# Optimization experiments

Hardware: AMD Instinct MI355X
Metric: run time of the kernel (lower is better)

## Reference

```python
import jax, jax.numpy as jnp
import numpy as np

N = 20000      # total nodes (20 proteins x 1000 residues)
E = 320000     # edges (avg degree 16)
F_IN = 22      # amino-acid feature dim
H = 4          # attention heads
C = 64         # hidden dim per head
HC = H * C     # 256
G = 20         # number of graphs
OUT = 128      # output embedding dim
NEG_SLOPE = 0.2


def setup_inputs() -> dict:
    key = jax.random.key(0)
    ks = jax.random.split(key, 24)
    x = jax.random.normal(ks[0], (N, F_IN), dtype=jnp.float32)
    edge_index = jax.random.randint(ks[1], (2, E), 0, N)
    batch = jnp.arange(N, dtype=jnp.int64) // (N // G)  # 1000 nodes per graph
    s = 0.1
    d = {
        'x': x, 'edge_index': edge_index, 'batch': batch,
        'Win': jax.random.normal(ks[2], (F_IN, C)) * s,
        'bin_': jnp.zeros((C,), jnp.float32),
        'Wout': jax.random.normal(ks[3], (2 * HC, OUT)) * s,
        'bout': jnp.zeros((OUT,), jnp.float32),
    }
    kidx = 4
    for i in range(3):
        in_dim = C if i == 0 else HC
        d[f'Wl{i}'] = jax.random.normal(ks[kidx], (in_dim, HC)) * s; kidx += 1
        d[f'Wr{i}'] = jax.random.normal(ks[kidx], (in_dim, HC)) * s; kidx += 1
        d[f'att{i}'] = jax.random.normal(ks[kidx], (H, C)) * s; kidx += 1
        d[f'b{i}'] = jnp.zeros((HC,), jnp.float32)
    return d


def _gatv2_layer(h, src, dst, Wl, Wr, att, bias):
    # PyG GATv2Conv (share_weights=False, concat=True), dropout off (eval)
    xl = (h @ Wl).reshape(-1, H, C)   # source transform (x_j)
    xr = (h @ Wr).reshape(-1, H, C)   # target transform (x_i)
    e = jax.nn.leaky_relu(xl[src] + xr[dst], NEG_SLOPE)  # [E+N, H, C]
    logit = jnp.einsum('ehc,hc->eh', e, att)             # [E+N, H]
    mx = jax.ops.segment_max(logit, dst, num_segments=N)
    mx = jnp.where(jnp.isfinite(mx), mx, 0.0)
    ex = jnp.exp(logit - mx[dst])
    den = jax.ops.segment_sum(ex, dst, num_segments=N)
    alpha = ex / (den[dst] + 1e-16)                      # segment softmax
    out = jax.ops.segment_sum(alpha[:, :, None] * xl[src], dst, num_segments=N)
    return out.reshape(-1, HC) + bias


def reference(x, edge_index, batch, Win, bin_,
              Wl0, Wr0, att0, b0, Wl1, Wr1, att1, b1, Wl2, Wr2, att2, b2,
              Wout, bout):
    # add self-loops once (add_self_loops=True in every GATv2Conv)
    loops = jnp.arange(N, dtype=edge_index.dtype)
    src = jnp.concatenate([edge_index[0], loops])
    dst = jnp.concatenate([edge_index[1], loops])

    h = jax.nn.relu(x @ Win + bin_)  # input_proj + ReLU (dropout = eval identity)
    layers = [(Wl0, Wr0, att0, b0), (Wl1, Wr1, att1, b1), (Wl2, Wr2, att2, b2)]
    for (Wl, Wr, att, b) in layers:
        h_prev = h
        h = jax.nn.elu(_gatv2_layer(h, src, dst, Wl, Wr, att, b))
        if h_prev.shape[-1] == h.shape[-1]:  # residual when dims match (layers 1,2)
            h = h + h_prev

    counts = jax.ops.segment_sum(jnp.ones((N,), h.dtype), batch, num_segments=G)
    x_mean = jax.ops.segment_sum(h, batch, num_segments=G) / counts[:, None]
    x_max = jax.ops.segment_max(h, batch, num_segments=G)
    x_global = jnp.concatenate([x_mean, x_max], axis=-1)  # [G, 512]
    return x_global @ Wout + bout                          # [G, 128]
```

## Files before the change

kernel.cpp:

```cpp
#include <hip/hip_runtime.h>
#include <hip/hip_bf16.h>
#include <math.h>

#define N_NODES 20000
#define N_EDGES 320000
#define F_IN 22
#define H_HEADS 4
#define C_DIM 64
#define HC 256
#define G_GRAPHS 20
#define OUT_DIM 128
#define NODES_PER_G 1000
#define ELL_CAP 64
#define SCAT_NB ((N_EDGES + 255) / 256)
#define INPROJ_NB (N_NODES / 4)

#if __has_builtin(__builtin_amdgcn_exp2f)
#define EXP2F __builtin_amdgcn_exp2f
#else
#define EXP2F exp2f
#endif

typedef unsigned short ushortT;
typedef __attribute__((ext_vector_type(8))) short short8;
typedef __attribute__((ext_vector_type(4))) float v4f;
typedef __attribute__((ext_vector_type(2))) float f2;

typedef const __attribute__((address_space(1))) void* gas_p;
typedef __attribute__((address_space(3))) void* las_p;

__device__ inline ushortT f2bf(float f) {
    unsigned int u = __float_as_uint(f);
    unsigned int r = (u + 0x7fffu + ((u >> 16) & 1u)) >> 16;
    return (ushortT)r;
}

__device__ inline unsigned int fkey(float f) {
    unsigned int u = __float_as_uint(f);
    return ((int)u < 0) ? ~u : (u | 0x80000000u);
}
__device__ inline float funkey(unsigned int k) {
    unsigned int u = (k & 0x80000000u) ? (k ^ 0x80000000u) : ~k;
    return __uint_as_float(u);
}

__global__ __launch_bounds__(256) void front_kernel(
        const int* __restrict__ esrc, const int* __restrict__ edst,
        int* __restrict__ fill, int* __restrict__ ell,
        const float* __restrict__ x, const float* __restrict__ Win,
        const float* __restrict__ bin, ushortT* __restrict__ h0b,
        const float* __restrict__ Wl0, const float* __restrict__ Wr0,
        const float* __restrict__ Wl1, const float* __restrict__ Wr1,
        const float* __restrict__ Wl2, const float* __restrict__ Wr2,
        ushortT* __restrict__ Bt0, ushortT* __restrict__ Bt1, ushortT* __restrict__ Bt2) {
    int tid = threadIdx.x;
    if (blockIdx.x < SCAT_NB) {
        int i = blockIdx.x * 256 + tid;
        if (i < N_EDGES) {
            int d = edst[i];
            int p = atomicAdd(&fill[d], 1);
            if (p < ELL_CAP) ell[(d << 6) + p] = esrc[i];
        }
        return;
    }
    if (blockIdx.x < SCAT_NB + INPROJ_NB) {
        int node = (blockIdx.x - SCAT_NB) * 4 + (tid >> 6);
        int c = tid & 63;
        float acc = bin[c];
        const float* xr = x + node * F_IN;
#pragma unroll
        for (int f = 0; f < F_IN; f++) acc += xr[f] * Win[f * C_DIM + c];
        h0b[node * C_DIM + c] = f2bf(acc > 0.f ? acc : 0.f);
        return;
    }
    int flat = blockIdx.x - SCAT_NB - INPROJ_NB;
    int z = flat >> 6;
    int rem = flat & 63;
    int kx = (rem >> 3) * 32;
    int nx = (rem & 7) * 32;
    int layer = z >> 1, isR = z & 1;
    const float* src; ushortT* dst; int K;
    if (layer == 0)      { K = 64;  dst = Bt0; src = isR ? Wr0 : Wl0; }
    else if (layer == 1) { K = 256; dst = Bt1; src = isR ? Wr1 : Wl1; }
    else                 { K = 256; dst = Bt2; src = isR ? Wr2 : Wl2; }
    if (kx >= K) return;
    __shared__ float tile[32][33];
    int c = tid & 31, r8 = tid >> 5;
#pragma unroll
    for (int i = 0; i < 4; i++) {
        int kk = r8 + i * 8;
        tile[kk][c] = src[(kx + kk) * 256 + nx + c];
    }
    __syncthreads();
    int nbase = isR ? 256 : 0;
#pragma unroll
    for (int i = 0; i < 4; i++) {
        int nn = r8 + i * 8;
        dst[(size_t)(nbase + nx + nn) * K + kx + c] = f2bf(tile[c][nn]);
    }
}

#define GBM 128
#define GBN 128
#define GBK 32

__global__ __launch_bounds__(256) void gemm_mfma_kernel(
        const ushortT* __restrict__ A, const ushortT* __restrict__ Bt,
        ushortT* __restrict__ XLb, ushortT* __restrict__ XRb, int M, int K) {
    __shared__ ushortT As[GBM * GBK];
    __shared__ ushortT Bs[GBN * GBK];
    int tid = threadIdx.x;
    int wave = tid >> 6, lane = tid & 63;
    int wm = wave & 1, wn = wave >> 1;
    int bm0 = blockIdx.y * GBM;
    int bn0 = blockIdx.x * GBN;

    v4f acc[4][4];
#pragma unroll
    for (int mt = 0; mt < 4; mt++)
#pragma unroll
        for (int nt = 0; nt < 4; nt++) acc[mt][nt] = (v4f){0.f, 0.f, 0.f, 0.f};

    int srow = lane >> 2;
    int scol = (lane & 3) * 8;
    int arow0 = wave * 16 + srow;
    int arow1 = arow0 + 64;
    int ag0 = bm0 + arow0; if (ag0 >= M) ag0 = 0;
    int ag1 = bm0 + arow1; if (ag1 >= M) ag1 = 0;
    const ushortT* aptr0 = A + (size_t)ag0 * K + scol;
    const ushortT* aptr1 = A + (size_t)ag1 * K + scol;
    const ushortT* bptr0 = Bt + (size_t)(bn0 + arow0) * K + scol;
    const ushortT* bptr1 = Bt + (size_t)(bn0 + arow1) * K + scol;
    las_p lA0 = (las_p)&As[(wave * 16) * GBK];
    las_p lA1 = (las_p)&As[(wave * 16 + 64) * GBK];
    las_p lB0 = (las_p)&Bs[(wave * 16) * GBK];
    las_p lB1 = (las_p)&Bs[(wave * 16 + 64) * GBK];

    int mrow = lane & 15;
    int koff = (lane >> 4) * 8;

    for (int k0 = 0; k0 < K; k0 += GBK) {
        __builtin_amdgcn_global_load_lds((gas_p)(aptr0 + k0), lA0, 16, 0, 0);
        __builtin_amdgcn_global_load_lds((gas_p)(aptr1 + k0), lA1, 16, 0, 0);
        __builtin_amdgcn_global_load_lds((gas_p)(bptr0 + k0), lB0, 16, 0, 0);
        __builtin_amdgcn_global_load_lds((gas_p)(bptr1 + k0), lB1, 16, 0, 0);
        __syncthreads();
        short8 af[4], bf[4];
#pragma unroll
        for (int mt = 0; mt < 4; mt++)
            af[mt] = *(const short8*)&As[(wm * 64 + mt * 16 + mrow) * GBK + koff];
#pragma unroll
        for (int nt = 0; nt < 4; nt++)
            bf[nt] = *(const short8*)&Bs[(wn * 64 + nt * 16 + mrow) * GBK + koff];
#pragma unroll
        for (int mt = 0; mt < 4; mt++)
#pragma unroll
            for (int nt = 0; nt < 4; nt++)
                acc[mt][nt] = __builtin_amdgcn_mfma_f32_16x16x32_bf16(af[mt], bf[nt], acc[mt][nt], 0, 0, 0);
        __syncthreads();
    }

    int cbase = bn0 + wn * 64;
    ushortT* dst = XLb;
    if (cbase >= 256) { dst = XRb; cbase -= 256; }
    int col = cbase + (lane & 15);
    int rbase = bm0 + wm * 64 + ((lane >> 4) * 4);
#pragma unroll
    for (int mt = 0; mt < 4; mt++) {
#pragma unroll
        for (int reg = 0; reg < 4; reg++) {
            int row = rbase + mt * 16 + reg;
            if (row < M) {
#pragma unroll
                for (int nt = 0; nt < 4; nt++)
                    dst[(size_t)row * 256 + col + nt * 16] = f2bf(acc[mt][nt][reg]);
            }
        }
    }
}

__device__ inline float row16_sum(float p) {
    p += __int_as_float(__builtin_amdgcn_update_dpp(0, __float_as_int(p), 0x121, 0xF, 0xF, false));
    p += __int_as_float(__builtin_amdgcn_update_dpp(0, __float_as_int(p), 0x122, 0xF, 0xF, false));
    p += __int_as_float(__builtin_amdgcn_update_dpp(0, __float_as_int(p), 0x124, 0xF, 0xF, false));
    p += __int_as_float(__builtin_amdgcn_update_dpp(0, __float_as_int(p), 0x128, 0xF, 0xF, false));
    return p;
}

__device__ inline void gat_edge(uint2 curu, f2 xr01, f2 xr23, f2 at01, f2 at23,
                                float live, float& den, f2& acc01, f2& acc23) {
    f2 x01, x23;
    x01.x = __uint_as_float(curu.x << 16);
    x01.y = __uint_as_float(curu.x & 0xffff0000u);
    x23.x = __uint_as_float(curu.y << 16);
    x23.y = __uint_as_float(curu.y & 0xffff0000u);
    f2 t01 = x01 + xr01;
    f2 t23 = x23 + xr23;
    t01 = __builtin_elementwise_max(t01, t01 * 0.2f);
    t23 = __builtin_elementwise_max(t23, t23 * 0.2f);
    f2 pp = t01 * at01;
    pp = __builtin_elementwise_fma(t23, at23, pp);
    float p = pp.x + pp.y;
    p = row16_sum(p);
    p = fminf(p, 110.f);
    float w = EXP2F(p) * live;
    den += w;
    f2 wv = {w, w};
    acc01 = __builtin_elementwise_fma(wv, x01, acc01);
    acc23 = __builtin_elementwise_fma(wv, x23, acc23);
}

__global__ __launch_bounds__(256) void gat_layer_kernel(
        const ushortT* __restrict__ xlb, const ushortT* __restrict__ xrb,
        const int* __restrict__ ell, const int* __restrict__ fill,
        const float* __restrict__ att, const float* __restrict__ bias,
        const float* __restrict__ hprev,
        float* __restrict__ hout, ushortT* __restrict__ houtb,
        float* __restrict__ psum, unsigned int* __restrict__ pmaxu) {
    int lane = threadIdx.x & 63;
    int wave = threadIdx.x >> 6;
    int d = blockIdx.x * 4 + wave;

    const uint2* xl2 = (const uint2*)xlb;
    uint2 xru = ((const uint2*)xrb)[d * 64 + lane];
    f2 xr01, xr23;
    xr01.x = __uint_as_float(xru.x << 16);
    xr01.y = __uint_as_float(xru.x & 0xffff0000u);
    xr23.x = __uint_as_float(xru.y << 16);
    xr23.y = __uint_as_float(xru.y & 0xffff0000u);

    float4 attv = ((const float4*)att)[lane];
    const float LOG2E = 1.44269504088896f;
    f2 at01 = {attv.x * LOG2E, attv.y * LOG2E};
    f2 at23 = {attv.z * LOG2E, attv.w * LOG2E};

    int deg = fill[d];
    if (deg > ELL_CAP - 1) deg = ELL_CAP - 1;
    int M = deg + 1;

    int idx = (lane < deg) ? ell[(d << 6) + lane] : d;

    float den = 0.f;
    f2 acc01 = {0.f, 0.f}, acc23 = {0.f, 0.f};

    uint2 buf[4];
#pragma unroll
    for (int k = 0; k < 4; k++) {
        int ni = __builtin_amdgcn_readlane(idx, k);
        buf[k] = xl2[(size_t)ni * 64 + lane];
    }
    int P = (M + 3) >> 2;
    for (int g = 0; g < P; g++) {
        int base = g * 4;
#pragma unroll
        for (int k = 0; k < 4; k++) {
            uint2 cur = buf[k];
            int ni = __builtin_amdgcn_readlane(idx, (base + 4 + k) & 63);
            buf[k] = xl2[(size_t)ni * 64 + lane];
            float live = (base + k < M) ? 1.0f : 0.0f;
            gat_edge(cur, xr01, xr23, at01, at23, live, den, acc01, acc23);
        }
    }

    float inv = 1.f / (den + 1e-16f);
    float4 bv = ((const float4*)bias)[lane];
    float4 v;
    v.x = acc01.x * inv + bv.x;
    v.y = acc01.y * inv + bv.y;
    v.z = acc23.x * inv + bv.z;
    v.w = acc23.y * inv + bv.w;
    v.x = v.x > 0.f ? v.x : __expf(v.x) - 1.f;
    v.y = v.y > 0.f ? v.y : __expf(v.y) - 1.f;
    v.z = v.z > 0.f ? v.z : __expf(v.z) - 1.f;
    v.w = v.w > 0.f ? v.w : __expf(v.w) - 1.f;
    if (hprev) {
        float4 hp = ((const float4*)hprev)[d * 64 + lane];
        v.x += hp.x; v.y += hp.y; v.z += hp.z; v.w += hp.w;
    }
    if (hout) ((float4*)hout)[d * 64 + lane] = v;
    if (houtb) {
        uint2 pb;
        pb.x = (unsigned int)f2bf(v.x) | ((unsigned int)f2bf(v.y) << 16);
        pb.y = (unsigned int)f2bf(v.z) | ((unsigned int)f2bf(v.w) << 16);
        ((uint2*)houtb)[d * 64 + lane] = pb;
    }
    if (psum) {
        __shared__ float4 red[4][64];
        red[wave][lane] = v;
        __syncthreads();
        if (wave == 0) {
            float4 a = red[0][lane], b = red[1][lane], c = red[2][lane], e = red[3][lane];
            float s0 = a.x + b.x + c.x + e.x;
            float s1 = a.y + b.y + c.y + e.y;
            float s2 = a.z + b.z + c.z + e.z;
            float s3 = a.w + b.w + c.w + e.w;
            float m0 = fmaxf(fmaxf(a.x, b.x), fmaxf(c.x, e.x));
            float m1 = fmaxf(fmaxf(a.y, b.y), fmaxf(c.y, e.y));
            float m2 = fmaxf(fmaxf(a.z, b.z), fmaxf(c.z, e.z));
            float m3 = fmaxf(fmaxf(a.w, b.w), fmaxf(c.w, e.w));
            int g = (blockIdx.x * 4) / NODES_PER_G;
            int cb = g * HC + lane * 4;
            atomicAdd(&psum[cb + 0], s0);
            atomicAdd(&psum[cb + 1], s1);
            atomicAdd(&psum[cb + 2], s2);
            atomicAdd(&psum[cb + 3], s3);
            atomicMax(&pmaxu[cb + 0], fkey(m0));
            atomicMax(&pmaxu[cb + 1], fkey(m1));
            atomicMax(&pmaxu[cb + 2], fkey(m2));
            atomicMax(&pmaxu[cb + 3], fkey(m3));
        }
    }
}

__global__ __launch_bounds__(256) void pool_out_kernel(
        const float* __restrict__ psum, const unsigned int* __restrict__ pmaxu,
        const float* __restrict__ Wout, const float* __restrict__ bout,
        float* __restrict__ out) {
    int g = blockIdx.x;
    int tid = threadIdx.x;
    __shared__ float xg[2 * HC];
    xg[tid] = psum[g * HC + tid] * (1.0f / NODES_PER_G);
    xg[HC + tid] = funkey(pmaxu[g * HC + tid]);
    __syncthreads();
    if (tid < OUT_DIM) {
        float acc = bout[tid];
        for (int j = 0; j < 2 * HC; j++) acc += xg[j] * Wout[j * OUT_DIM + tid];
        out[g * OUT_DIM + tid] = acc;
    }
}


extern "C" void kernel_launch(void* const* d_in, const int* in_sizes, int n_in,
                              void* d_out, int out_size, void* d_ws, size_t ws_size,
                              hipStream_t stream) {
    const float* x    = (const float*)d_in[0];
    const int*   ei   = (const int*)d_in[1];
    const float* Win  = (const float*)d_in[3];
    const float* bin  = (const float*)d_in[4];
    const float* Wout = (const float*)d_in[5];
    const float* bout = (const float*)d_in[6];
    const float* Wl[3] = {(const float*)d_in[7],  (const float*)d_in[11], (const float*)d_in[15]};
    const float* Wr[3] = {(const float*)d_in[8],  (const float*)d_in[12], (const float*)d_in[16]};
    const float* att[3] = {(const float*)d_in[9], (const float*)d_in[13], (const float*)d_in[17]};
    const float* bb[3] = {(const float*)d_in[10], (const float*)d_in[14], (const float*)d_in[18]};
    float* out = (float*)d_out;

    const int* esrc = ei;
    const int* edst = ei + N_EDGES;

    float* hA   = (float*)d_ws;
    float* hB   = hA + (size_t)N_NODES * HC;
    int* fill   = (int*)(hB + (size_t)N_NODES * HC);
    float* psum = (float*)(fill + N_NODES);
    unsigned int* pmaxu = (unsigned int*)(psum + G_GRAPHS * HC);
    ushortT* h0b = (ushortT*)(pmaxu + G_GRAPHS * HC);
    ushortT* hAb = h0b + (size_t)N_NODES * C_DIM;
    ushortT* hBb = hAb + (size_t)N_NODES * HC;
    ushortT* XLb = hBb + (size_t)N_NODES * HC;
    ushortT* XRb = XLb + (size_t)N_NODES * HC;
    ushortT* Bt0 = XRb + (size_t)N_NODES * HC;
    ushortT* Bt1 = Bt0 + 512 * 64;
    ushortT* Bt2 = Bt1 + 512 * 256;
    int* ell   = (int*)(Bt2 + 512 * 256);

    (void)hipMemsetAsync(fill, 0,
        N_NODES * sizeof(int) + 2 * G_GRAPHS * HC * sizeof(float), stream);

    front_kernel<<<SCAT_NB + INPROJ_NB + 384, 256, 0, stream>>>(
        esrc, edst, fill, ell, x, Win, bin, h0b,
        Wl[0], Wr[0], Wl[1], Wr[1], Wl[2], Wr[2], Bt0, Bt1, Bt2);

    dim3 ggrid(512 / GBN, (N_NODES + GBM - 1) / GBM);

    gemm_mfma_kernel<<<ggrid, 256, 0, stream>>>(h0b, Bt0, XLb, XRb, N_NODES, C_DIM);
    gat_layer_kernel<<<N_NODES / 4, 256, 0, stream>>>(XLb, XRb, ell, fill, att[0], bb[0],
                                                      nullptr, hA, hAb, nullptr, nullptr);

    gemm_mfma_kernel<<<ggrid, 256, 0, stream>>>(hAb, Bt1, XLb, XRb, N_NODES, HC);
    gat_layer_kernel<<<N_NODES / 4, 256, 0, stream>>>(XLb, XRb, ell, fill, att[1], bb[1],
                                                      hA, hB, hBb, nullptr, nullptr);

    gemm_mfma_kernel<<<ggrid, 256, 0, stream>>>(hBb, Bt2, XLb, XRb, N_NODES, HC);
    gat_layer_kernel<<<N_NODES / 4, 256, 0, stream>>>(XLb, XRb, ell, fill, att[2], bb[2],
                                                      hB, nullptr, nullptr, psum, pmaxu);

    pool_out_kernel<<<G_GRAPHS, 256, 0, stream>>>(psum, pmaxu, Wout, bout, out);
}
```

Baseline: 310.5 us.

## Deepen GAT gather prefetch, use ds_swizzle reductions, slice pooling atomics

The GAT layer kernel now keeps two banks of four prefetched source rows in flight instead of one, so more gather latency is hidden per wave. The 16-lane logit reduction switches from DPP row shifts to ds_swizzle butterfly patterns. Pooling atomics are spread across 8 slices per graph, and the output kernel reduces those slices, which lowers contention on the same addresses. The costs are more registers for the prefetch buffers, possible lower occupancy, the LDS-path latency of swizzle compared with DPP, and extra over-fetch past the degree.

After: 291.8 us. 1.06x faster.

```diff
diff --git a/kernel.cpp b/kernel.cpp
--- a/kernel.cpp
+++ b/kernel.cpp
@@ -11,6 +11,7 @@
 #define G_GRAPHS 20
 #define OUT_DIM 128
 #define NODES_PER_G 1000
+#define P_SLICES 8
 #define ELL_CAP 64
 #define SCAT_NB ((N_EDGES + 255) / 256)
 #define INPROJ_NB (N_NODES / 4)
@@ -179,12 +180,9 @@
     }
 }
 
-__device__ inline float row16_sum(float p) {
-    p += __int_as_float(__builtin_amdgcn_update_dpp(0, __float_as_int(p), 0x121, 0xF, 0xF, false));
-    p += __int_as_float(__builtin_amdgcn_update_dpp(0, __float_as_int(p), 0x122, 0xF, 0xF, false));
-    p += __int_as_float(__builtin_amdgcn_update_dpp(0, __float_as_int(p), 0x124, 0xF, 0xF, false));
-    p += __int_as_float(__builtin_amdgcn_update_dpp(0, __float_as_int(p), 0x128, 0xF, 0xF, false));
-    return p;
+template <int PAT>
+__device__ inline float swz_add(float p) {
+    return p + __int_as_float(__builtin_amdgcn_ds_swizzle(__float_as_int(p), PAT));
 }
 
 __device__ inline void gat_edge(uint2 curu, f2 xr01, f2 xr23, f2 at01, f2 at23,
@@ -201,7 +199,10 @@
     f2 pp = t01 * at01;
     pp = __builtin_elementwise_fma(t23, at23, pp);
     float p = pp.x + pp.y;
-    p = row16_sum(p);
+    p = swz_add<0x041F>(p);
+    p = swz_add<0x081F>(p);
+    p = swz_add<0x101F>(p);
+    p = swz_add<0x201F>(p);
     p = fminf(p, 110.f);
     float w = EXP2F(p) * live;
     den += w;
@@ -243,22 +244,38 @@
     float den = 0.f;
     f2 acc01 = {0.f, 0.f}, acc23 = {0.f, 0.f};
 
-    uint2 buf[4];
+    uint2 bufA[4], bufB[4];
 #pragma unroll
     for (int k = 0; k < 4; k++) {
         int ni = __builtin_amdgcn_readlane(idx, k);
-        buf[k] = xl2[(size_t)ni * 64 + lane];
+        bufA[k] = xl2[(size_t)ni * 64 + lane];
+    }
+#pragma unroll
+    for (int k = 0; k < 4; k++) {
+        int ni = __builtin_amdgcn_readlane(idx, 4 + k);
+        bufB[k] = xl2[(size_t)ni * 64 + lane];
     }
     int P = (M + 3) >> 2;
-    for (int g = 0; g < P; g++) {
+    for (int g = 0; g < P; g += 2) {
         int base = g * 4;
 #pragma unroll
         for (int k = 0; k < 4; k++) {
-            uint2 cur = buf[k];
-            int ni = __builtin_amdgcn_readlane(idx, (base + 4 + k) & 63);
-            buf[k] = xl2[(size_t)ni * 64 + lane];
+            uint2 cur = bufA[k];
+            int ni = __builtin_amdgcn_readlane(idx, (base + 8 + k) & 63);
+            bufA[k] = xl2[(size_t)ni * 64 + lane];
             float live = (base + k < M) ? 1.0f : 0.0f;
             gat_edge(cur, xr01, xr23, at01, at23, live, den, acc01, acc23);
+        }
+        if (g + 1 < P) {
+            int b2 = base + 4;
+#pragma unroll
+            for (int k = 0; k < 4; k++) {
+                uint2 cur = bufB[k];
+                int ni = __builtin_amdgcn_readlane(idx, (b2 + 8 + k) & 63);
+                bufB[k] = xl2[(size_t)ni * 64 + lane];
+                float live = (b2 + k < M) ? 1.0f : 0.0f;
+                gat_edge(cur, xr01, xr23, at01, at23, live, den, acc01, acc23);
+            }
         }
     }
 
@@ -299,7 +316,8 @@
             float m2 = fmaxf(fmaxf(a.z, b.z), fmaxf(c.z, e.z));
             float m3 = fmaxf(fmaxf(a.w, b.w), fmaxf(c.w, e.w));
             int g = (blockIdx.x * 4) / NODES_PER_G;
-            int cb = g * HC + lane * 4;
+            int slice = blockIdx.x & (P_SLICES - 1);
+            int cb = (slice * G_GRAPHS + g) * HC + lane * 4;
             atomicAdd(&psum[cb + 0], s0);
             atomicAdd(&psum[cb + 1], s1);
             atomicAdd(&psum[cb + 2], s2);
@@ -319,8 +337,14 @@
     int g = blockIdx.x;
     int tid = threadIdx.x;
     __shared__ float xg[2 * HC];
-    xg[tid] = psum[g * HC + tid] * (1.0f / NODES_PER_G);
-    xg[HC + tid] = funkey(pmaxu[g * HC + tid]);
+    float sum = 0.f, mx = -INFINITY;
+#pragma unroll
+    for (int s = 0; s < P_SLICES; s++) {
+        sum += psum[(s * G_GRAPHS + g) * HC + tid];
+        mx = fmaxf(mx, funkey(pmaxu[(s * G_GRAPHS + g) * HC + tid]));
+    }
+    xg[tid] = sum * (1.0f / NODES_PER_G);
+    xg[HC + tid] = mx;
     __syncthreads();
     if (tid < OUT_DIM) {
         float acc = bout[tid];
@@ -352,8 +376,8 @@
     float* hB   = hA + (size_t)N_NODES * HC;
     int* fill   = (int*)(hB + (size_t)N_NODES * HC);
     float* psum = (float*)(fill + N_NODES);
-    unsigned int* pmaxu = (unsigned int*)(psum + G_GRAPHS * HC);
-    ushortT* h0b = (ushortT*)(pmaxu + G_GRAPHS * HC);
+    unsigned int* pmaxu = (unsigned int*)(psum + (size_t)P_SLICES * G_GRAPHS * HC);
+    ushortT* h0b = (ushortT*)(pmaxu + (size_t)P_SLICES * G_GRAPHS * HC);
     ushortT* hAb = h0b + (size_t)N_NODES * C_DIM;
     ushortT* hBb = hAb + (size_t)N_NODES * HC;
     ushortT* XLb = hBb + (size_t)N_NODES * HC;
@@ -364,7 +388,8 @@
     int* ell   = (int*)(Bt2 + 512 * 256);
 
     (void)hipMemsetAsync(fill, 0,
-        N_NODES * sizeof(int) + 2 * G_GRAPHS * HC * sizeof(float), stream);
+        N_NODES * sizeof(int) + 2 * (size_t)P_SLICES * G_GRAPHS * HC * sizeof(float),
+        stream);
 
     front_kernel<<<SCAT_NB + INPROJ_NB + 384, 256, 0, stream>>>(
         esrc, edst, fill, ell, x, Win, bin, h0b,
```
